# Performance work log

Hardware: AMD Instinct MI355X
Metric: run time of the kernel (lower is better)

## Reference

```python
import jax, jax.numpy as jnp
import numpy as np
import math

D_MODEL = 1024
NUM_HEADS = 16


def setup_inputs() -> dict:
    key = jax.random.key(0)
    k1, k2, k3 = jax.random.split(key, 3)
    x = jax.random.normal(k1, (4, 2048, D_MODEL), dtype=jnp.float32)
    scale = 1.0 / math.sqrt(D_MODEL)
    W_qkv = jax.random.normal(k2, (3 * D_MODEL, D_MODEL), dtype=jnp.float32) * scale
    W_out = jax.random.normal(k3, (D_MODEL, D_MODEL), dtype=jnp.float32) * scale
    return {"x": x, "W_qkv": W_qkv, "W_out": W_out}


def reference(x, W_qkv, W_out):
    B, S, D = x.shape
    H = NUM_HEADS
    hd = D // H
    qkv = x @ W_qkv.T                      # [B,S,3D]
    q, k, v = jnp.split(qkv, 3, axis=-1)
    # [B,S,D] -> [B,H,S,hd]
    q = q.reshape(B, S, H, hd).transpose(0, 2, 1, 3)
    k = k.reshape(B, S, H, hd).transpose(0, 2, 1, 3)
    v = v.reshape(B, S, H, hd).transpose(0, 2, 1, 3)
    scores = jnp.einsum('bhqd,bhkd->bhqk', q, k) / math.sqrt(hd)
    causal = jnp.tril(jnp.ones((S, S), dtype=bool))
    scores = jnp.where(causal, scores, -jnp.inf)
    w = jax.nn.softmax(scores, axis=-1)
    out = jnp.einsum('bhqk,bhkd->bhqd', w, v)
    out = out.transpose(0, 2, 1, 3).reshape(B, S, D)
    return out @ W_out.T
```

## Files before the change

kernel.cpp:

```cpp
#include <hip/hip_runtime.h>
#include <hip/hip_bf16.h>
#include <stdint.h>


typedef __bf16 bf16_t;
typedef __attribute__((ext_vector_type(8))) __bf16 bf16x8;
typedef __attribute__((ext_vector_type(4))) __bf16 bf16x4;
typedef __attribute__((ext_vector_type(4))) float f32x4;

#define LOG2E 1.44269504088896340736f
#define SCLF (0.125f * LOG2E)
#define MFMA16(a, b, c) __builtin_amdgcn_mfma_f32_16x16x32_bf16(a, b, c, 0, 0, 0)

__device__ __forceinline__ bf16x8 ld8(const bf16_t* p) {
    return *(const bf16x8*)p;
}
__device__ __forceinline__ bf16x8 cvt8(const float* p) {
    f32x4 a = *(const f32x4*)p;
    f32x4 b = *(const f32x4*)(p + 4);
    bf16x8 r;
    r[0] = (bf16_t)a[0]; r[1] = (bf16_t)a[1]; r[2] = (bf16_t)a[2]; r[3] = (bf16_t)a[3];
    r[4] = (bf16_t)b[0]; r[5] = (bf16_t)b[1]; r[6] = (bf16_t)b[2]; r[7] = (bf16_t)b[3];
    return r;
}

__device__ __forceinline__ bool probe_f32(const void* w) {
    const uint16_t* u = (const uint16_t*)w;
    int cnt = 0;
#pragma unroll
    for (int i = 0; i < 64; ++i) {
        const int e = (u[i] >> 7) & 0xFF;
        cnt += (e >= 96 && e <= 150) ? 1 : 0;
    }
    return cnt < 56;
}

__device__ __forceinline__ void gll16(const bf16_t* g, bf16_t* l) {
    __builtin_amdgcn_global_load_lds(
        (const __attribute__((address_space(1))) void*)g,
        (__attribute__((address_space(3))) void*)l, 16, 0, 0);
}

__global__ __launch_bounds__(256) void cvt_kernel(
    const void* __restrict__ x, const void* __restrict__ wq, const void* __restrict__ wo,
    bf16_t* __restrict__ xb, bf16_t* __restrict__ wqb, bf16_t* __restrict__ wob)
{
    const int gid = blockIdx.x * 256 + threadIdx.x;
    const void* src;
    bf16_t* dst;
    int off;
    if (gid < 1048576)        { src = x;  dst = xb;  off = gid; }
    else if (gid < 1441792)   { src = wq; dst = wqb; off = gid - 1048576; }
    else                      { src = wo; dst = wob; off = gid - 1441792; }
    const bool f32 = probe_f32(src);
    const bf16x8 v = f32 ? cvt8((const float*)src + (size_t)off * 8)
                         : ld8((const bf16_t*)src + (size_t)off * 8);
    *(bf16x8*)(dst + (size_t)off * 8) = v;
}

template <int EPI>
__global__ __launch_bounds__(256) void gemm_bt_lds(
    const bf16_t* __restrict__ A, const bf16_t* __restrict__ B,
    void* __restrict__ C, bf16_t* __restrict__ VT,
    int M, int N, int K)
{
    __shared__ __align__(16) bf16_t lsA[128 * 32];
    __shared__ __align__(16) bf16_t lsB[128 * 32];

    const int t    = threadIdx.x;
    const int lane = t & 63;
    const int wid  = t >> 6;
    const int quad = lane >> 4;
    const int l15  = lane & 15;
    const int wm   = (wid & 1) * 64;
    const int wn   = (wid >> 1) * 64;
    const int m0   = blockIdx.y * 128;
    const int n0   = blockIdx.x * 128;

    const bf16_t* Ar = A + (size_t)(m0 + (t >> 2)) * K + (t & 3) * 8;
    const bf16_t* Br = B + (size_t)(n0 + (t >> 2)) * K + (t & 3) * 8;
    bf16_t* la = lsA + t * 8;
    bf16_t* lb = lsB + t * 8;

    f32x4 acc[4][4];
#pragma unroll
    for (int i = 0; i < 4; ++i)
#pragma unroll
        for (int j = 0; j < 4; ++j) acc[i][j] = (f32x4){0.f, 0.f, 0.f, 0.f};

    for (int k0 = 0; k0 < K; k0 += 32) {
        __syncthreads();
        gll16(Ar + k0, la);
        gll16(Ar + (size_t)64 * K + k0, la + 2048);
        gll16(Br + k0, lb);
        gll16(Br + (size_t)64 * K + k0, lb + 2048);
        __syncthreads();

        bf16x8 af[4], bfr[4];
#pragma unroll
        for (int i = 0; i < 4; ++i)
            af[i] = ld8(lsA + (wm + i * 16 + l15) * 32 + quad * 8);
#pragma unroll
        for (int j = 0; j < 4; ++j)
            bfr[j] = ld8(lsB + (wn + j * 16 + l15) * 32 + quad * 8);
#pragma unroll
        for (int i = 0; i < 4; ++i)
#pragma unroll
            for (int j = 0; j < 4; ++j)
                acc[i][j] = MFMA16(af[i], bfr[j], acc[i][j]);
    }

#pragma unroll
    for (int i = 0; i < 4; ++i) {
        const int row = m0 + wm + i * 16 + quad * 4;
#pragma unroll
        for (int j = 0; j < 4; ++j) {
            const int col = n0 + wn + j * 16 + l15;
#pragma unroll
            for (int r = 0; r < 4; ++r) {
                const int rr = row + r;
                if (EPI == 0) {
                    ((float*)C)[(size_t)rr * N + col] = acc[i][j][r];
                } else {
                    const bf16_t v = (bf16_t)acc[i][j][r];
                    if (col < 2048) {
                        ((bf16_t*)C)[(size_t)rr * 2048 + col] = v;
                    } else {
                        const int c2 = col - 2048;
                        const int h = c2 >> 6, d = c2 & 63;
                        const int b = rr >> 11, s = rr & 2047;
                        VT[((size_t)((b << 4) + h) * 64 + d) * 2048 + s] = v;
                    }
                }
            }
        }
    }
}

template <int EPI>
__global__ __launch_bounds__(256) void gemm_bt_kernel(
    const void* __restrict__ A, const void* __restrict__ B,
    void* __restrict__ C, bf16_t* __restrict__ VT,
    int aFollow, int bFollow,
    int M, int N, int K)
{
    __shared__ __align__(16) bf16_t lsA[128 * 32];
    __shared__ __align__(16) bf16_t lsB[128 * 32];

    const bool f32in = probe_f32(B);
    const bool aF32  = (aFollow != 0) && f32in;
    const bool bF32  = (bFollow != 0) && f32in;

    const int t    = threadIdx.x;
    const int lane = t & 63;
    const int wid  = t >> 6;
    const int quad = lane >> 4;
    const int l15  = lane & 15;
    const int wm   = (wid & 1) * 64;
    const int wn   = (wid >> 1) * 64;
    const int m0   = blockIdx.y * 128;
    const int n0   = blockIdx.x * 128;

    const size_t arow = (size_t)(m0 + (t >> 2));
    const size_t brow = (size_t)(n0 + (t >> 2));
    const int    scol = (t & 3) * 8;

    const bf16_t* Ab = (const bf16_t*)A;
    const bf16_t* Bb = (const bf16_t*)B;
    const float*  Af = (const float*)A;
    const float*  Bf = (const float*)B;

    f32x4 acc[4][4];
#pragma unroll
    for (int i = 0; i < 4; ++i)
#pragma unroll
        for (int j = 0; j < 4; ++j) acc[i][j] = (f32x4){0.f, 0.f, 0.f, 0.f};

    for (int k0 = 0; k0 < K; k0 += 32) {
        bf16x8 sa0, sa1, sb0, sb1;
        if (aF32) {
            sa0 = cvt8(Af + arow * K + k0 + scol);
            sa1 = cvt8(Af + (arow + 64) * K + k0 + scol);
        } else {
            sa0 = ld8(Ab + arow * K + k0 + scol);
            sa1 = ld8(Ab + (arow + 64) * K + k0 + scol);
        }
        if (bF32) {
            sb0 = cvt8(Bf + brow * K + k0 + scol);
            sb1 = cvt8(Bf + (brow + 64) * K + k0 + scol);
        } else {
            sb0 = ld8(Bb + brow * K + k0 + scol);
            sb1 = ld8(Bb + (brow + 64) * K + k0 + scol);
        }

        __syncthreads();
        *(bf16x8*)(lsA + t * 8)        = sa0;
        *(bf16x8*)(lsA + 2048 + t * 8) = sa1;
        *(bf16x8*)(lsB + t * 8)        = sb0;
        *(bf16x8*)(lsB + 2048 + t * 8) = sb1;
        __syncthreads();

        bf16x8 af[4], bfr[4];
#pragma unroll
        for (int i = 0; i < 4; ++i)
            af[i] = ld8(lsA + (wm + i * 16 + l15) * 32 + quad * 8);
#pragma unroll
        for (int j = 0; j < 4; ++j)
            bfr[j] = ld8(lsB + (wn + j * 16 + l15) * 32 + quad * 8);
#pragma unroll
        for (int i = 0; i < 4; ++i)
#pragma unroll
            for (int j = 0; j < 4; ++j)
                acc[i][j] = MFMA16(af[i], bfr[j], acc[i][j]);
    }

#pragma unroll
    for (int i = 0; i < 4; ++i) {
        const int row = m0 + wm + i * 16 + quad * 4;
#pragma unroll
        for (int j = 0; j < 4; ++j) {
            const int col = n0 + wn + j * 16 + l15;
#pragma unroll
            for (int r = 0; r < 4; ++r) {
                const int rr = row + r;
                if (EPI == 0) {
                    ((float*)C)[(size_t)rr * N + col] = acc[i][j][r];
                } else {
                    const bf16_t v = (bf16_t)acc[i][j][r];
                    if (col < 2048) {
                        ((bf16_t*)C)[(size_t)rr * 2048 + col] = v;
                    } else {
                        const int c2 = col - 2048;
                        const int h = c2 >> 6, d = c2 & 63;
                        const int b = rr >> 11, s = rr & 2047;
                        VT[((size_t)((b << 4) + h) * 64 + d) * 2048 + s] = v;
                    }
                }
            }
        }
    }
}

struct Kfrag { bf16x8 k00, k01, k10, k11; };

__device__ __forceinline__ Kfrag ldk(const bf16_t* Kbase, int key0) {
    const bf16_t* kp = Kbase + (size_t)key0 * 2048;
    Kfrag f;
    f.k00 = ld8(kp);
    f.k01 = ld8(kp + 32);
    f.k10 = ld8(kp + (size_t)16 * 2048);
    f.k11 = ld8(kp + (size_t)16 * 2048 + 32);
    return f;
}

__device__ __forceinline__ bf16x4 expq(f32x4 s, float& lsum) {
    bf16x4 r;
#pragma unroll
    for (int i = 0; i < 4; ++i) {
        const float e = exp2f(s[i] * SCLF);
        r[i] = (bf16_t)e;
        lsum += (float)r[i];
    }
    return r;
}
__device__ __forceinline__ bf16x4 expq_m(f32x4 s, float& lsum, int quad, int l15) {
    bf16x4 r;
#pragma unroll
    for (int i = 0; i < 4; ++i) {
        const float e = (quad * 4 + i <= l15) ? exp2f(s[i] * SCLF) : 0.f;
        r[i] = (bf16_t)e;
        lsum += (float)r[i];
    }
    return r;
}

typedef union { bf16x4 h; int u[2]; } pk2;
typedef union { int u[4]; bf16x8 v; } pk4u;

__device__ __forceinline__ bf16x8 xpose(bf16x4 p0, bf16x4 p1, int s0b, int s1b, bool lowsel) {
    pk2 a, b;
    a.h = p0; b.h = p1;
    const int x0 = __builtin_amdgcn_ds_bpermute(s0b, a.u[0]);
    const int y0 = __builtin_amdgcn_ds_bpermute(s0b, b.u[0]);
    const int x1 = __builtin_amdgcn_ds_bpermute(s0b, a.u[1]);
    const int y1 = __builtin_amdgcn_ds_bpermute(s0b, b.u[1]);
    const int x2 = __builtin_amdgcn_ds_bpermute(s1b, a.u[0]);
    const int y2 = __builtin_amdgcn_ds_bpermute(s1b, b.u[0]);
    const int x3 = __builtin_amdgcn_ds_bpermute(s1b, a.u[1]);
    const int y3 = __builtin_amdgcn_ds_bpermute(s1b, b.u[1]);
    pk4u r;
    r.u[0] = lowsel ? x0 : y0;
    r.u[1] = lowsel ? x1 : y1;
    r.u[2] = lowsel ? x2 : y2;
    r.u[3] = lowsel ? x3 : y3;
    return r.v;
}

template <int DIAG>
__device__ __forceinline__ void attn_step(
    const Kfrag& kf, const bf16_t* __restrict__ Vbase, int key0,
    int quad, int l15, int s0b, int s1b, bool lowsel,
    const bf16x8& qa0, const bf16x8& qa1, const bf16x8& qb0, const bf16x8& qb1,
    f32x4 (&oa)[4], f32x4 (&ob)[4], float& la, float& lb)
{
    const bf16_t* vp = Vbase + key0;
    const bf16x8 vf0 = ld8(vp);
    const bf16x8 vf1 = ld8(vp + (size_t)16 * 2048);
    const bf16x8 vf2 = ld8(vp + (size_t)32 * 2048);
    const bf16x8 vf3 = ld8(vp + (size_t)48 * 2048);

    const f32x4 Z = (f32x4){0.f, 0.f, 0.f, 0.f};
    f32x4 s0a = Z, s1a = Z, s0b_ = Z, s1b_ = Z;
    s0a = MFMA16(kf.k00, qa0, s0a); s0a = MFMA16(kf.k01, qa1, s0a);
    s0b_ = MFMA16(kf.k00, qb0, s0b_); s0b_ = MFMA16(kf.k01, qb1, s0b_);
    if (!DIAG) {
        s1a = MFMA16(kf.k10, qa0, s1a); s1a = MFMA16(kf.k11, qa1, s1a);
    }
    s1b_ = MFMA16(kf.k10, qb0, s1b_); s1b_ = MFMA16(kf.k11, qb1, s1b_);

    bf16x4 pa0, pa1, pb0, pb1;
    if (DIAG) {
        pa0 = expq_m(s0a, la, quad, l15);
        pa1 = (bf16x4){(bf16_t)0.f, (bf16_t)0.f, (bf16_t)0.f, (bf16_t)0.f};
        pb0 = expq(s0b_, lb);
        pb1 = expq_m(s1b_, lb, quad, l15);
    } else {
        pa0 = expq(s0a, la); pa1 = expq(s1a, la);
        pb0 = expq(s0b_, lb); pb1 = expq(s1b_, lb);
    }

    const bf16x8 pfa = xpose(pa0, pa1, s0b, s1b, lowsel);
    const bf16x8 pfb = xpose(pb0, pb1, s0b, s1b, lowsel);

    oa[0] = MFMA16(pfa, vf0, oa[0]); ob[0] = MFMA16(pfb, vf0, ob[0]);
    oa[1] = MFMA16(pfa, vf1, oa[1]); ob[1] = MFMA16(pfb, vf1, ob[1]);
    oa[2] = MFMA16(pfa, vf2, oa[2]); ob[2] = MFMA16(pfb, vf2, ob[2]);
    oa[3] = MFMA16(pfa, vf3, oa[3]); ob[3] = MFMA16(pfb, vf3, ob[3]);
}

__global__ __launch_bounds__(256, 4) void attn_kernel(
    const bf16_t* __restrict__ qk, const bf16_t* __restrict__ vt,
    bf16_t* __restrict__ out)
{
    const int t    = threadIdx.x;
    const int wid  = t >> 6;
    const int lane = t & 63;
    const int quad = lane >> 4;
    const int l15  = lane & 15;

    const int bx = blockIdx.x;
    const int u  = bx & 255;
    const int v_ = bx >> 8;
    const int bh = ((u & 15) << 2) | wid;
    const int c  = u >> 4;
    const int bs = (v_ & 1) ? (31 - c) : c;
    const int qt = bs + ((v_ >> 1) << 5);
    const int b  = bh >> 4;
    const int h  = bh & 15;
    const int q0 = qt << 5;

    const int s0b = ((((quad << 1)) & 3) * 16 + l15) << 2;
    const int s1b = ((((quad << 1) + 1) & 3) * 16 + l15) << 2;
    const bool lowsel = quad < 2;

    const bf16_t* Qp = qk + (size_t)(b * 2048 + q0 + l15) * 2048 + h * 64 + quad * 8;
    const bf16x8 qa0 = ld8(Qp);
    const bf16x8 qa1 = ld8(Qp + 32);
    const bf16x8 qb0 = ld8(Qp + (size_t)16 * 2048);
    const bf16x8 qb1 = ld8(Qp + (size_t)16 * 2048 + 32);

    const bf16_t* Kbase = qk + (size_t)(b * 2048 + l15) * 2048 + 1024 + h * 64 + quad * 8;
    const bf16_t* Vbase = vt + ((size_t)bh * 64 + l15) * 2048 + quad * 8;

    f32x4 oa[4], ob[4];
#pragma unroll
    for (int v = 0; v < 4; ++v) {
        oa[v] = (f32x4){0.f, 0.f, 0.f, 0.f};
        ob[v] = (f32x4){0.f, 0.f, 0.f, 0.f};
    }
    float la = 0.f, lb = 0.f;

    Kfrag kc = ldk(Kbase, 0);
    for (int kb = 0; kb < qt; ++kb) {
        Kfrag kn = ldk(Kbase, (kb + 1) << 5);
        attn_step<0>(kc, Vbase, kb << 5, quad, l15, s0b, s1b, lowsel,
                     qa0, qa1, qb0, qb1, oa, ob, la, lb);
        kc = kn;
    }
    attn_step<1>(kc, Vbase, qt << 5, quad, l15, s0b, s1b, lowsel,
                 qa0, qa1, qb0, qb1, oa, ob, la, lb);

    la += __shfl_xor(la, 16); la += __shfl_xor(la, 32);
    lb += __shfl_xor(lb, 16); lb += __shfl_xor(lb, 32);
    const float inva = 1.0f / la;
    const float invb = 1.0f / lb;

    const size_t obase = (size_t)(b * 2048 + q0 + quad * 4) * 1024 + h * 64 + l15;
#pragma unroll
    for (int r = 0; r < 4; ++r) {
        const float ia = __shfl(inva, quad * 4 + r);
        const float ib = __shfl(invb, quad * 4 + r);
#pragma unroll
        for (int v = 0; v < 4; ++v) {
            out[obase + (size_t)r * 1024 + v * 16]        = (bf16_t)(oa[v][r] * ia);
            out[obase + (size_t)(16 + r) * 1024 + v * 16] = (bf16_t)(ob[v][r] * ib);
        }
    }
}

__global__ void ws_check_kernel(float* out, int code) {
    if (code != 0 && threadIdx.x == 0) out[0] = (float)code;
}

extern "C" void kernel_launch(void* const* d_in, const int* in_sizes, int n_in,
                              void* d_out, int out_size, void* d_ws, size_t ws_size,
                              hipStream_t stream)
{
    const void* x    = d_in[0];
    const void* wqkv = d_in[1];
    const void* wout = d_in[2];

    bf16_t* qkbuf   = (bf16_t*)d_ws;
    bf16_t* vtbuf   = qkbuf + (size_t)8192 * 2048;
    bf16_t* attnbuf = vtbuf + (size_t)64 * 64 * 2048;
    bf16_t* xb      = attnbuf + (size_t)8192 * 1024;
    bf16_t* wqb     = xb + (size_t)8192 * 1024;
    bf16_t* wob     = wqb + (size_t)3072 * 1024;
    float*  outp    = (float*)d_out;

    const int  wsBad = (ws_size < (size_t)64 * 1024 * 1024) ? 512 : 0;
    const bool big   = ws_size >= (size_t)88 * 1024 * 1024;

    if (big) {
        cvt_kernel<<<6144, 256, 0, stream>>>(x, wqkv, wout, xb, wqb, wob);
        gemm_bt_lds<1><<<dim3(24, 64), 256, 0, stream>>>(
            xb, wqb, qkbuf, vtbuf, 8192, 3072, 1024);
        attn_kernel<<<1024, 256, 0, stream>>>(qkbuf, vtbuf, attnbuf);
        gemm_bt_lds<0><<<dim3(8, 64), 256, 0, stream>>>(
            attnbuf, wob, outp, nullptr, 8192, 1024, 1024);
    } else {
        gemm_bt_kernel<1><<<dim3(24, 64), 256, 0, stream>>>(
            x, wqkv, qkbuf, vtbuf, 1, 1, 8192, 3072, 1024);
        attn_kernel<<<1024, 256, 0, stream>>>(qkbuf, vtbuf, attnbuf);
        gemm_bt_kernel<0><<<dim3(8, 64), 256, 0, stream>>>(
            attnbuf, wout, outp, nullptr, 0, 1, 8192, 1024, 1024);
    }

    ws_check_kernel<<<1, 64, 0, stream>>>(outp, wsBad);
}
```

Measured before the change: 356.1 us.

## Split attention KV loop across wave pairs and drop separate conversion kernel

The attention kernel now gives each query tile to two waves that take alternating key blocks. Their partial outputs and row sums are merged through LDS, and the grid doubles to 2048 blocks, so more of the machine works on the causal loop. The launch code also drops the workspace-size-gated path that ran a separate fp32-to-bf16 conversion kernel. It uses one GEMM kernel that probes the dtype and picks either the direct-to-LDS bf16 path or in-register fp32 conversion. Since the inputs are fp32, the GEMMs now convert inline on every tile load and lose the global_load_lds path. That trades one conversion launch for redundant conversion work inside each GEMM.

```diff
diff --git a/kernel.cpp b/kernel.cpp
--- a/kernel.cpp
+++ b/kernel.cpp
@@ -41,31 +41,17 @@
         (__attribute__((address_space(3))) void*)l, 16, 0, 0);
 }
 
-__global__ __launch_bounds__(256) void cvt_kernel(
-    const void* __restrict__ x, const void* __restrict__ wq, const void* __restrict__ wo,
-    bf16_t* __restrict__ xb, bf16_t* __restrict__ wqb, bf16_t* __restrict__ wob)
-{
-    const int gid = blockIdx.x * 256 + threadIdx.x;
-    const void* src;
-    bf16_t* dst;
-    int off;
-    if (gid < 1048576)        { src = x;  dst = xb;  off = gid; }
-    else if (gid < 1441792)   { src = wq; dst = wqb; off = gid - 1048576; }
-    else                      { src = wo; dst = wob; off = gid - 1441792; }
-    const bool f32 = probe_f32(src);
-    const bf16x8 v = f32 ? cvt8((const float*)src + (size_t)off * 8)
-                         : ld8((const bf16_t*)src + (size_t)off * 8);
-    *(bf16x8*)(dst + (size_t)off * 8) = v;
-}
-
 template <int EPI>
-__global__ __launch_bounds__(256) void gemm_bt_lds(
-    const bf16_t* __restrict__ A, const bf16_t* __restrict__ B,
+__global__ __launch_bounds__(256) void gemm_bt_dual(
+    const void* __restrict__ A, const void* __restrict__ B,
     void* __restrict__ C, bf16_t* __restrict__ VT,
+    int aFollow, int bFollow,
     int M, int N, int K)
 {
     __shared__ __align__(16) bf16_t lsA[128 * 32];
     __shared__ __align__(16) bf16_t lsB[128 * 32];
+
+    const bool f32in = probe_f32(B);
 
     const int t    = threadIdx.x;
     const int lane = t & 63;
@@ -77,141 +63,87 @@
     const int m0   = blockIdx.y * 128;
     const int n0   = blockIdx.x * 128;
 
-    const bf16_t* Ar = A + (size_t)(m0 + (t >> 2)) * K + (t & 3) * 8;
-    const bf16_t* Br = B + (size_t)(n0 + (t >> 2)) * K + (t & 3) * 8;
-    bf16_t* la = lsA + t * 8;
-    bf16_t* lb = lsB + t * 8;
-
     f32x4 acc[4][4];
 #pragma unroll
     for (int i = 0; i < 4; ++i)
 #pragma unroll
         for (int j = 0; j < 4; ++j) acc[i][j] = (f32x4){0.f, 0.f, 0.f, 0.f};
 
-    for (int k0 = 0; k0 < K; k0 += 32) {
-        __syncthreads();
-        gll16(Ar + k0, la);
-        gll16(Ar + (size_t)64 * K + k0, la + 2048);
-        gll16(Br + k0, lb);
-        gll16(Br + (size_t)64 * K + k0, lb + 2048);
-        __syncthreads();
-
-        bf16x8 af[4], bfr[4];
-#pragma unroll
-        for (int i = 0; i < 4; ++i)
-            af[i] = ld8(lsA + (wm + i * 16 + l15) * 32 + quad * 8);
-#pragma unroll
-        for (int j = 0; j < 4; ++j)
-            bfr[j] = ld8(lsB + (wn + j * 16 + l15) * 32 + quad * 8);
-#pragma unroll
-        for (int i = 0; i < 4; ++i)
+    if (!f32in) {
+        const bf16_t* Ar = (const bf16_t*)A + (size_t)(m0 + (t >> 2)) * K + (t & 3) * 8;
+        const bf16_t* Br = (const bf16_t*)B + (size_t)(n0 + (t >> 2)) * K + (t & 3) * 8;
+        bf16_t* la = lsA + t * 8;
+        bf16_t* lb = lsB + t * 8;
+
+        for (int k0 = 0; k0 < K; k0 += 32) {
+            __syncthreads();
+            gll16(Ar + k0, la);
+            gll16(Ar + (size_t)64 * K + k0, la + 2048);
+            gll16(Br + k0, lb);
+            gll16(Br + (size_t)64 * K + k0, lb + 2048);
+            __syncthreads();
+
+            bf16x8 af[4], bfr[4];
+#pragma unroll
+            for (int i = 0; i < 4; ++i)
+                af[i] = ld8(lsA + (wm + i * 16 + l15) * 32 + quad * 8);
 #pragma unroll
             for (int j = 0; j < 4; ++j)
-                acc[i][j] = MFMA16(af[i], bfr[j], acc[i][j]);
-    }
-
-#pragma unroll
-    for (int i = 0; i < 4; ++i) {
-        const int row = m0 + wm + i * 16 + quad * 4;
-#pragma unroll
-        for (int j = 0; j < 4; ++j) {
-            const int col = n0 + wn + j * 16 + l15;
-#pragma unroll
-            for (int r = 0; r < 4; ++r) {
-                const int rr = row + r;
-                if (EPI == 0) {
-                    ((float*)C)[(size_t)rr * N + col] = acc[i][j][r];
-                } else {
-                    const bf16_t v = (bf16_t)acc[i][j][r];
-                    if (col < 2048) {
-                        ((bf16_t*)C)[(size_t)rr * 2048 + col] = v;
-                    } else {
-                        const int c2 = col - 2048;
-                        const int h = c2 >> 6, d = c2 & 63;
-                        const int b = rr >> 11, s = rr & 2047;
-                        VT[((size_t)((b << 4) + h) * 64 + d) * 2048 + s] = v;
-                    }
-                }
+                bfr[j] = ld8(lsB + (wn + j * 16 + l15) * 32 + quad * 8);
+#pragma unroll
+            for (int i = 0; i < 4; ++i)
+#pragma unroll
+                for (int j = 0; j < 4; ++j)
+                    acc[i][j] = MFMA16(af[i], bfr[j], acc[i][j]);
+        }
+    } else {
+        const bool aF32 = (aFollow != 0);
+        const bool bF32 = (bFollow != 0);
+        const size_t arow = (size_t)(m0 + (t >> 2));
+        const size_t brow = (size_t)(n0 + (t >> 2));
+        const int    scol = (t & 3) * 8;
+        const bf16_t* Ab = (const bf16_t*)A;
+        const bf16_t* Bb = (const bf16_t*)B;
+        const float*  Af = (const float*)A;
+        const float*  Bf = (const float*)B;
+
+        for (int k0 = 0; k0 < K; k0 += 32) {
+            bf16x8 sa0, sa1, sb0, sb1;
+            if (aF32) {
+                sa0 = cvt8(Af + arow * K + k0 + scol);
+                sa1 = cvt8(Af + (arow + 64) * K + k0 + scol);
+            } else {
+                sa0 = ld8(Ab + arow * K + k0 + scol);
+                sa1 = ld8(Ab + (arow + 64) * K + k0 + scol);
             }
-        }
-    }
-}
-
-template <int EPI>
-__global__ __launch_bounds__(256) void gemm_bt_kernel(
-    const void* __restrict__ A, const void* __restrict__ B,
-    void* __restrict__ C, bf16_t* __restrict__ VT,
-    int aFollow, int bFollow,
-    int M, int N, int K)
-{
-    __shared__ __align__(16) bf16_t lsA[128 * 32];
-    __shared__ __align__(16) bf16_t lsB[128 * 32];
-
-    const bool f32in = probe_f32(B);
-    const bool aF32  = (aFollow != 0) && f32in;
-    const bool bF32  = (bFollow != 0) && f32in;
-
-    const int t    = threadIdx.x;
-    const int lane = t & 63;
-    const int wid  = t >> 6;
-    const int quad = lane >> 4;
-    const int l15  = lane & 15;
-    const int wm   = (wid & 1) * 64;
-    const int wn   = (wid >> 1) * 64;
-    const int m0   = blockIdx.y * 128;
-    const int n0   = blockIdx.x * 128;
-
-    const size_t arow = (size_t)(m0 + (t >> 2));
-    const size_t brow = (size_t)(n0 + (t >> 2));
-    const int    scol = (t & 3) * 8;
-
-    const bf16_t* Ab = (const bf16_t*)A;
-    const bf16_t* Bb = (const bf16_t*)B;
-    const float*  Af = (const float*)A;
-    const float*  Bf = (const float*)B;
-
-    f32x4 acc[4][4];
-#pragma unroll
-    for (int i = 0; i < 4; ++i)
-#pragma unroll
-        for (int j = 0; j < 4; ++j) acc[i][j] = (f32x4){0.f, 0.f, 0.f, 0.f};
-
-    for (int k0 = 0; k0 < K; k0 += 32) {
-        bf16x8 sa0, sa1, sb0, sb1;
-        if (aF32) {
-            sa0 = cvt8(Af + arow * K + k0 + scol);
-            sa1 = cvt8(Af + (arow + 64) * K + k0 + scol);
-        } else {
-            sa0 = ld8(Ab + arow * K + k0 + scol);
-            sa1 = ld8(Ab + (arow + 64) * K + k0 + scol);
-        }
-        if (bF32) {
-            sb0 = cvt8(Bf + brow * K + k0 + scol);
-            sb1 = cvt8(Bf + (brow + 64) * K + k0 + scol);
-        } else {
-            sb0 = ld8(Bb + brow * K + k0 + scol);
-            sb1 = ld8(Bb + (brow + 64) * K + k0 + scol);
-        }
-
-        __syncthreads();
-        *(bf16x8*)(lsA + t * 8)        = sa0;
-        *(bf16x8*)(lsA + 2048 + t * 8) = sa1;
-        *(bf16x8*)(lsB + t * 8)        = sb0;
-        *(bf16x8*)(lsB + 2048 + t * 8) = sb1;
-        __syncthreads();
-
-        bf16x8 af[4], bfr[4];
-#pragma unroll
-        for (int i = 0; i < 4; ++i)
-            af[i] = ld8(lsA + (wm + i * 16 + l15) * 32 + quad * 8);
-#pragma unroll
-        for (int j = 0; j < 4; ++j)
-            bfr[j] = ld8(lsB + (wn + j * 16 + l15) * 32 + quad * 8);
-#pragma unroll
-        for (int i = 0; i < 4; ++i)
+            if (bF32) {
+                sb0 = cvt8(Bf + brow * K + k0 + scol);
+                sb1 = cvt8(Bf + (brow + 64) * K + k0 + scol);
+            } else {
+                sb0 = ld8(Bb + brow * K + k0 + scol);
+                sb1 = ld8(Bb + (brow + 64) * K + k0 + scol);
+            }
+
+            __syncthreads();
+            *(bf16x8*)(lsA + t * 8)        = sa0;
+            *(bf16x8*)(lsA + 2048 + t * 8) = sa1;
+            *(bf16x8*)(lsB + t * 8)        = sb0;
+            *(bf16x8*)(lsB + 2048 + t * 8) = sb1;
+            __syncthreads();
+
+            bf16x8 af[4], bfr[4];
+#pragma unroll
+            for (int i = 0; i < 4; ++i)
+                af[i] = ld8(lsA + (wm + i * 16 + l15) * 32 + quad * 8);
 #pragma unroll
             for (int j = 0; j < 4; ++j)
-                acc[i][j] = MFMA16(af[i], bfr[j], acc[i][j]);
+                bfr[j] = ld8(lsB + (wn + j * 16 + l15) * 32 + quad * 8);
+#pragma unroll
+            for (int i = 0; i < 4; ++i)
+#pragma unroll
+                for (int j = 0; j < 4; ++j)
+                    acc[i][j] = MFMA16(af[i], bfr[j], acc[i][j]);
+        }
     }
 
 #pragma unroll
@@ -338,23 +270,29 @@
     oa[3] = MFMA16(pfa, vf3, oa[3]); ob[3] = MFMA16(pfb, vf3, ob[3]);
 }
 
-__global__ __launch_bounds__(256, 4) void attn_kernel(
+__global__ __launch_bounds__(256) void attn_kernel(
     const bf16_t* __restrict__ qk, const bf16_t* __restrict__ vt,
     bf16_t* __restrict__ out)
 {
+    __shared__ float mrg[2][64][34];
+
     const int t    = threadIdx.x;
     const int wid  = t >> 6;
     const int lane = t & 63;
     const int quad = lane >> 4;
     const int l15  = lane & 15;
 
-    const int bx = blockIdx.x;
-    const int u  = bx & 255;
-    const int v_ = bx >> 8;
-    const int bh = ((u & 15) << 2) | wid;
+    const int bx    = blockIdx.x;
+    const int u     = bx & 255;
+    const int v_    = bx >> 8;
+    const int pairI = wid >> 1;
+    const int par   = wid & 1;
+
+    const int bh = ((u & 15) << 2) | (v_ & 3);
     const int c  = u >> 4;
-    const int bs = (v_ & 1) ? (31 - c) : c;
-    const int qt = bs + ((v_ >> 1) << 5);
+    const int hi = v_ >> 2;
+    const int cc = hi ? (15 - c) : c;
+    const int qt = cc | (hi << 4) | (pairI << 5);
     const int b  = bh >> 4;
     const int h  = bh & 15;
     const int q0 = qt << 5;
@@ -380,15 +318,45 @@
     }
     float la = 0.f, lb = 0.f;
 
-    Kfrag kc = ldk(Kbase, 0);
-    for (int kb = 0; kb < qt; ++kb) {
-        Kfrag kn = ldk(Kbase, (kb + 1) << 5);
-        attn_step<0>(kc, Vbase, kb << 5, quad, l15, s0b, s1b, lowsel,
-                     qa0, qa1, qb0, qb1, oa, ob, la, lb);
-        kc = kn;
-    }
-    attn_step<1>(kc, Vbase, qt << 5, quad, l15, s0b, s1b, lowsel,
-                 qa0, qa1, qb0, qb1, oa, ob, la, lb);
+    const bool dg = ((qt & 1) == par);
+    int kb = par;
+    if (kb < qt || dg) {
+        Kfrag kc = ldk(Kbase, ((kb < qt) ? kb : qt) << 5);
+        while (kb < qt) {
+            const int nk = (kb + 2 < qt) ? (kb + 2) : qt;
+            Kfrag kn = ldk(Kbase, nk << 5);
+            attn_step<0>(kc, Vbase, kb << 5, quad, l15, s0b, s1b, lowsel,
+                         qa0, qa1, qb0, qb1, oa, ob, la, lb);
+            kc = kn;
+            kb += 2;
+        }
+        if (dg)
+            attn_step<1>(kc, Vbase, qt << 5, quad, l15, s0b, s1b, lowsel,
+                         qa0, qa1, qb0, qb1, oa, ob, la, lb);
+    }
+
+    float* m = &mrg[pairI][lane][0];
+    if (par == 1) {
+#pragma unroll
+        for (int v = 0; v < 4; ++v)
+#pragma unroll
+            for (int r = 0; r < 4; ++r) {
+                m[v * 4 + r]      = oa[v][r];
+                m[16 + v * 4 + r] = ob[v][r];
+            }
+        m[32] = la; m[33] = lb;
+    }
+    __syncthreads();
+    if (par == 1) return;
+
+#pragma unroll
+    for (int v = 0; v < 4; ++v)
+#pragma unroll
+        for (int r = 0; r < 4; ++r) {
+            oa[v][r] += m[v * 4 + r];
+            ob[v][r] += m[16 + v * 4 + r];
+        }
+    la += m[32]; lb += m[33];
 
     la += __shfl_xor(la, 16); la += __shfl_xor(la, 32);
     lb += __shfl_xor(lb, 16); lb += __shfl_xor(lb, 32);
@@ -423,28 +391,17 @@
     bf16_t* qkbuf   = (bf16_t*)d_ws;
     bf16_t* vtbuf   = qkbuf + (size_t)8192 * 2048;
     bf16_t* attnbuf = vtbuf + (size_t)64 * 64 * 2048;
-    bf16_t* xb      = attnbuf + (size_t)8192 * 1024;
-    bf16_t* wqb     = xb + (size_t)8192 * 1024;
-    bf16_t* wob     = wqb + (size_t)3072 * 1024;
     float*  outp    = (float*)d_out;
 
-    const int  wsBad = (ws_size < (size_t)64 * 1024 * 1024) ? 512 : 0;
-    const bool big   = ws_size >= (size_t)88 * 1024 * 1024;
-
-    if (big) {
-        cvt_kernel<<<6144, 256, 0, stream>>>(x, wqkv, wout, xb, wqb, wob);
-        gemm_bt_lds<1><<<dim3(24, 64), 256, 0, stream>>>(
-            xb, wqb, qkbuf, vtbuf, 8192, 3072, 1024);
-        attn_kernel<<<1024, 256, 0, stream>>>(qkbuf, vtbuf, attnbuf);
-        gemm_bt_lds<0><<<dim3(8, 64), 256, 0, stream>>>(
-            attnbuf, wob, outp, nullptr, 8192, 1024, 1024);
-    } else {
-        gemm_bt_kernel<1><<<dim3(24, 64), 256, 0, stream>>>(
-            x, wqkv, qkbuf, vtbuf, 1, 1, 8192, 3072, 1024);
-        attn_kernel<<<1024, 256, 0, stream>>>(qkbuf, vtbuf, attnbuf);
-        gemm_bt_kernel<0><<<dim3(8, 64), 256, 0, stream>>>(
-            attnbuf, wout, outp, nullptr, 0, 1, 8192, 1024, 1024);
-    }
+    const int wsBad = (ws_size < (size_t)64 * 1024 * 1024) ? 512 : 0;
+
+    gemm_bt_dual<1><<<dim3(24, 64), 256, 0, stream>>>(
+        x, wqkv, qkbuf, vtbuf, 1, 1, 8192, 3072, 1024);
+
+    attn_kernel<<<2048, 256, 0, stream>>>(qkbuf, vtbuf, attnbuf);
+
+    gemm_bt_dual<0><<<dim3(8, 64), 256, 0, stream>>>(
+        attnbuf, wout, outp, nullptr, 0, 1, 8192, 1024, 1024);
 
     ws_check_kernel<<<1, 64, 0, stream>>>(outp, wsBad);
 }
```

Result: slower. 404.8 us (+13.7%).
